# Kernel optimization log

Hardware: AMD Instinct MI355X
Metric: run time of the kernel (lower is better)

Reference implementation:

```python
import jax, jax.numpy as jnp
import numpy as np

B, CIN, H, W = 4, 128, 64, 64
PL, ATT, R = 256, 64, 16   # planes, planes//4, MD_R
STEPS = 6                   # TRAIN_STEPS default
EPS = 1e-6


def _l2norm(v, axis):
    return v / jnp.maximum(jnp.linalg.norm(v, axis=axis, keepdims=True), 1e-12)


def setup_inputs() -> dict:
    key = jax.random.key(0)
    ks = jax.random.split(key, 11)
    s = 0.05
    return {
        "x": jax.random.normal(ks[0], (B, CIN, H, W), jnp.float32),
        "conv1_w": jax.random.normal(ks[1], (PL, CIN), jnp.float32) * s,      # 1x1 conv, no bias
        "conv3_w": jax.random.normal(ks[2], (PL, 1, 3, 3), jnp.float32) * s,  # depthwise 3x3
        "conv3_b": jax.random.normal(ks[3], (PL,), jnp.float32) * s,
        "lower_w": jax.random.normal(ks[4], (PL, PL), jnp.float32) * s,       # Conv1d k=1
        "lower_b": jax.random.normal(ks[5], (PL,), jnp.float32) * s,
        "ca1_w": jax.random.normal(ks[6], (ATT, PL), jnp.float32) * s,        # channel attn 1x1
        "ca2_w": jax.random.normal(ks[7], (PL, ATT), jnp.float32) * s,
        "fc_w": jax.random.normal(ks[8], (CIN, PL), jnp.float32) * s,         # fc_adapt_channels1
        "fc_b": jax.random.normal(ks[9], (CIN,), jnp.float32) * s,
        "bases_init": jax.random.uniform(ks[10], (B * H * W, 1, R), jnp.float32),  # rand_init bases
    }


def reference(x, conv1_w, conv3_w, conv3_b, lower_w, lower_b, ca1_w, ca2_w, fc_w, fc_b, bases_init):
    # conv1 (1x1, no bias) then depthwise 3x3 (groups=PL)
    y = jnp.einsum('bchw,oc->bohw', x, conv1_w)
    y = jax.lax.conv_general_dilated(y, conv3_w, (1, 1), 'SAME',
                                     dimension_numbers=('NCHW', 'OIHW', 'NCHW'),
                                     feature_group_count=PL)
    y = y + conv3_b[None, :, None, None]
    # '(b s) c h w -> (b h w) c s' with s=1 -> tokens [M, C]
    xm = jnp.transpose(y, (0, 2, 3, 1)).reshape(B * H * W, PL)
    # Hamburger lower_bread: Conv1d(k=1) + ReLU
    xl = jax.nn.relu(xm @ lower_w.T + lower_b)
    xn = xl[:, None, :]                        # NMF x: [M, D=1, N=C]
    # NMF2D local_inference (torch.no_grad in original)
    xs = jax.lax.stop_gradient(xn)
    bases = _l2norm(bases_init, 1)             # [M, 1, R]
    coef = jax.nn.softmax(jnp.einsum('mdn,mdr->mnr', xs, bases), axis=-1)  # inv_t=1
    for _ in range(STEPS):
        num = jnp.einsum('mdn,mdr->mnr', xs, bases)
        den = jnp.einsum('mnr,mrk->mnk', coef, jnp.einsum('mdr,mdk->mrk', bases, bases))
        coef = coef * num / (den + EPS)
        num = jnp.einsum('mdn,mnr->mdr', xs, coef)
        den = jnp.einsum('mdr,mrk->mdk', bases, jnp.einsum('mnr,mnk->mrk', coef, coef))
        bases = bases * num / (den + EPS)
    bases = jax.lax.stop_gradient(bases)
    coef = jax.lax.stop_gradient(coef)
    # compute_coef (differentiable via xn)
    num = jnp.einsum('mdn,mdr->mnr', xn, bases)
    den = jnp.einsum('mnr,mrk->mnk', coef, jnp.einsum('mdr,mdk->mrk', bases, bases))
    coef = coef * num / (den + EPS)
    xr = jnp.einsum('mdr,mnr->mn', bases, coef)     # bases @ coef^T, [M, C] (D=1 squeezed)
    feat = jax.nn.relu(xm + xr)                     # Hamburger residual + ReLU
    # mean over s (s=1) and back to [B, C, H, W]
    feat = jnp.transpose(feat.reshape(B, H, W, PL), (0, 3, 1, 2))
    # AMPooling channel attention
    avg = feat.mean(axis=(2, 3))
    mx = feat.max(axis=(2, 3))
    ca = lambda v: jax.nn.relu(v @ ca1_w.T) @ ca2_w.T
    att = jax.nn.sigmoid(ca(avg) + ca(mx))          # [B, C]
    out = feat * att[:, :, None, None]
    out = jnp.einsum('bchw,oc->bohw', out, fc_w) + fc_b[None, :, None, None]
    return out, att[:, :, None, None]
```

## Files before the change

kernel.cpp:

```cpp
#include <hip/hip_runtime.h>
#include <hip/hip_bf16.h>
#include <math.h>

#define EPS 1e-6f
#define PITCH 72

typedef short s16x8 __attribute__((ext_vector_type(8)));
typedef float f32x4 __attribute__((ext_vector_type(4)));

__device__ __forceinline__ short bf16of(float f) {
  __hip_bfloat16 h = __float2bfloat16(f);
  return __builtin_bit_cast(short, h);
}
__device__ __forceinline__ float f32of(unsigned short u) {
  unsigned int x = ((unsigned int)u) << 16;
  return __builtin_bit_cast(float, x);
}

__global__ __launch_bounds__(256) void k_conv1x1(const float* __restrict__ x,
                                                 const float* __restrict__ w1,
                                                 short* __restrict__ ybf) {
  __shared__ __align__(16) short Aw[256 * PITCH];
  __shared__ __align__(16) short Xs[64 * PITCH];
  const int t = threadIdx.x;
  const int m0 = blockIdx.x * 64;
  const int img = m0 >> 12, hw0 = m0 & 4095;
  const int lane = t & 63, w = t >> 6;
  const int lrow = lane & 15, lk = (lane >> 4) * 8;
  f32x4 acc[8][2];
#pragma unroll
  for (int i = 0; i < 8; ++i)
#pragma unroll
    for (int j = 0; j < 2; ++j) acc[i][j] = {0.f, 0.f, 0.f, 0.f};

  for (int kk = 0; kk < 128; kk += 64) {
    __syncthreads();
    {
      const float* wp = w1 + (size_t)t * 128 + kk;
#pragma unroll
      for (int q = 0; q < 16; ++q) {
        const float4 v = *(const float4*)(wp + q * 4);
        short4 sv = {bf16of(v.x), bf16of(v.y), bf16of(v.z), bf16of(v.w)};
        *(short4*)(&Aw[t * PITCH + q * 4]) = sv;
      }
    }
    {
      const int m4 = (t & 15) * 4;
      const int cg = (t >> 4) * 4;
      float4 col[4];
#pragma unroll
      for (int cc = 0; cc < 4; ++cc)
        col[cc] = *(const float4*)(x + (size_t)(img * 128 + kk + cg + cc) * 4096 + hw0 + m4);
#pragma unroll
      for (int r = 0; r < 4; ++r) {
        short4 sv = {bf16of(((const float*)&col[0])[r]),
                     bf16of(((const float*)&col[1])[r]),
                     bf16of(((const float*)&col[2])[r]),
                     bf16of(((const float*)&col[3])[r])};
        *(short4*)(&Xs[(m4 + r) * PITCH + cg]) = sv;
      }
    }
    __syncthreads();
#pragma unroll
    for (int ks = 0; ks < 2; ++ks) {
      const int ko = ks * 32 + lk;
      s16x8 bfr[2];
#pragma unroll
      for (int j = 0; j < 2; ++j)
        bfr[j] = *(const s16x8*)(&Xs[(((w >> 1) * 2 + j) * 16 + lrow) * PITCH + ko]);
#pragma unroll
      for (int i = 0; i < 8; ++i) {
        const s16x8 af = *(const s16x8*)(&Aw[(((w & 1) * 8 + i) * 16 + lrow) * PITCH + ko]);
#pragma unroll
        for (int j = 0; j < 2; ++j)
          acc[i][j] = __builtin_amdgcn_mfma_f32_16x16x32_bf16(af, bfr[j], acc[i][j], 0, 0, 0);
      }
    }
  }
#pragma unroll
  for (int i = 0; i < 8; ++i) {
    const int p = ((w & 1) * 8 + i) * 16 + (lane >> 4) * 4;
#pragma unroll
    for (int j = 0; j < 2; ++j) {
      const int m = m0 + ((w >> 1) * 2 + j) * 16 + lrow;
      const f32x4 v = acc[i][j];
      short4 sv = {bf16of(v.x), bf16of(v.y), bf16of(v.z), bf16of(v.w)};
      *(short4*)(ybf + (size_t)m * 256 + p) = sv;
    }
  }
}

__global__ __launch_bounds__(256) void k_dwconv(const unsigned short* __restrict__ ybf,
                                                const float* __restrict__ w3,
                                                const float* __restrict__ b3,
                                                float* __restrict__ xm) {
  __shared__ float wt[9][256];
  __shared__ float bs[256];
  const int t = threadIdx.x;
#pragma unroll
  for (int i = 0; i < 9; ++i) wt[i][t] = w3[t * 9 + i];
  bs[t] = b3[t];
  __syncthreads();
  const int sub = t >> 6;
  const int pq = t & 63;
  const int m = blockIdx.x * 4 + sub;
  const int hw = m & 4095;
  const int h = hw >> 6, ww = hw & 63;
  const int bb = m >> 12;
  float4 acc = *(const float4*)(&bs[pq * 4]);
#pragma unroll
  for (int dy = -1; dy <= 1; ++dy) {
    const int hh = h + dy;
    if (hh < 0 || hh > 63) continue;
#pragma unroll
    for (int dx = -1; dx <= 1; ++dx) {
      const int w2 = ww + dx;
      if (w2 < 0 || w2 > 63) continue;
      const int idx = (dy + 1) * 3 + (dx + 1);
      const ushort4 v =
          *(const ushort4*)(ybf + (size_t)((bb << 12) + (hh << 6) + w2) * 256 + pq * 4);
      const float4 wv = *(const float4*)(&wt[idx][pq * 4]);
      acc.x += f32of(v.x) * wv.x;
      acc.y += f32of(v.y) * wv.y;
      acc.z += f32of(v.z) * wv.z;
      acc.w += f32of(v.w) * wv.w;
    }
  }
  *(float4*)(xm + (size_t)m * 256 + pq * 4) = acc;
}

__global__ __launch_bounds__(256) void k_lower(const float* __restrict__ xm,
                                               const float* __restrict__ lw,
                                               const float* __restrict__ lb,
                                               float* __restrict__ xl) {
  __shared__ __align__(16) short Aw[256 * PITCH];
  __shared__ __align__(16) short Xs[64 * PITCH];
  const int t = threadIdx.x;
  const int m0 = blockIdx.x * 64;
  const int lane = t & 63, w = t >> 6;
  const int lrow = lane & 15, lk = (lane >> 4) * 8;
  f32x4 acc[8][2];
#pragma unroll
  for (int i = 0; i < 8; ++i)
#pragma unroll
    for (int j = 0; j < 2; ++j) acc[i][j] = {0.f, 0.f, 0.f, 0.f};

  for (int kk = 0; kk < 256; kk += 64) {
    __syncthreads();
    {
      const float* wp = lw + (size_t)t * 256 + kk;
#pragma unroll
      for (int q = 0; q < 16; ++q) {
        const float4 v = *(const float4*)(wp + q * 4);
        short4 sv = {bf16of(v.x), bf16of(v.y), bf16of(v.z), bf16of(v.w)};
        *(short4*)(&Aw[t * PITCH + q * 4]) = sv;
      }
    }
    {
      const int m = t & 63, q = t >> 6;
      const float* xp = xm + (size_t)(m0 + m) * 256 + kk + q * 16;
#pragma unroll
      for (int jj = 0; jj < 4; ++jj) {
        const float4 v = *(const float4*)(xp + jj * 4);
        short4 sv = {bf16of(v.x), bf16of(v.y), bf16of(v.z), bf16of(v.w)};
        *(short4*)(&Xs[m * PITCH + q * 16 + jj * 4]) = sv;
      }
    }
    __syncthreads();
#pragma unroll
    for (int ks = 0; ks < 2; ++ks) {
      const int ko = ks * 32 + lk;
      s16x8 bfr[2];
#pragma unroll
      for (int j = 0; j < 2; ++j)
        bfr[j] = *(const s16x8*)(&Xs[(((w >> 1) * 2 + j) * 16 + lrow) * PITCH + ko]);
#pragma unroll
      for (int i = 0; i < 8; ++i) {
        const s16x8 af = *(const s16x8*)(&Aw[(((w & 1) * 8 + i) * 16 + lrow) * PITCH + ko]);
#pragma unroll
        for (int j = 0; j < 2; ++j)
          acc[i][j] = __builtin_amdgcn_mfma_f32_16x16x32_bf16(af, bfr[j], acc[i][j], 0, 0, 0);
      }
    }
  }
#pragma unroll
  for (int i = 0; i < 8; ++i) {
    const int n = ((w & 1) * 8 + i) * 16 + (lane >> 4) * 4;
    const float4 bias = *(const float4*)(lb + n);
#pragma unroll
    for (int j = 0; j < 2; ++j) {
      const int m = m0 + ((w >> 1) * 2 + j) * 16 + lrow;
      f32x4 v = acc[i][j];
      v.x = fmaxf(v.x + bias.x, 0.f);
      v.y = fmaxf(v.y + bias.y, 0.f);
      v.z = fmaxf(v.z + bias.z, 0.f);
      v.w = fmaxf(v.w + bias.w, 0.f);
      *(f32x4*)(xl + (size_t)m * 256 + n) = v;
    }
  }
}

__global__ __launch_bounds__(256) void k_em_fast(const float* __restrict__ xl,
                                                 const float* __restrict__ binit,
                                                 const float* __restrict__ xm,
                                                 short* __restrict__ featb,
                                                 float* __restrict__ psum,
                                                 float* __restrict__ pmax,
                                                 int* __restrict__ flag) {
  __shared__ float psL[1024], pmL[1024];
  __shared__ int sflag;
  const int t = threadIdx.x;
  const int lane = t & 63, w = t >> 6;
  const int bid = blockIdx.x;
  const int m0 = bid * 16 + w * 4;
  bool asym = false;
#pragma unroll
  for (int p = 0; p < 4; ++p) {
    const float bv = binit[(size_t)(m0 + p) * 16 + (lane & 15)];
    const float bn = bv / fmaxf(fabsf(bv), 1e-12f);
    asym |= !__all(bn == 1.0f);
  }
  if (t == 0) sflag = 0;
  __syncthreads();
  if (asym && lane == 0) sflag = 1;
  __syncthreads();
  if (sflag) {
    if (t == 0) flag[bid] = 1;
    return;
  }

  float s[4][4], C[4][4], Bv[4];
#pragma unroll
  for (int p = 0; p < 4; ++p) {
    const f32x4 s4 = *(const f32x4*)(xl + (size_t)(m0 + p) * 256 + lane * 4);
    s[p][0] = s4.x;
    s[p][1] = s4.y;
    s[p][2] = s4.z;
    s[p][3] = s4.w;
    Bv[p] = 1.f;
#pragma unroll
    for (int i = 0; i < 4; ++i) C[p][i] = 0.0625f;
  }
  for (int step = 0; step < 6; ++step) {
    float pnum[4], psq[4];
#pragma unroll
    for (int p = 0; p < 4; ++p) {
      const float k1 = 16.f * Bv[p] * Bv[p];
      pnum[p] = 0.f;
      psq[p] = 0.f;
#pragma unroll
      for (int i = 0; i < 4; ++i) {
        const float den = fmaf(C[p][i], k1, EPS);
        const float cn = C[p][i] * (s[p][i] * Bv[p]) * __builtin_amdgcn_rcpf(den);
        C[p][i] = cn;
        pnum[p] = fmaf(s[p][i], cn, pnum[p]);
        psq[p] = fmaf(cn, cn, psq[p]);
      }
    }
#pragma unroll
    for (int d = 1; d < 64; d <<= 1) {
#pragma unroll
      for (int p = 0; p < 4; ++p) {
        pnum[p] += __shfl_xor(pnum[p], d, 64);
        psq[p] += __shfl_xor(psq[p], d, 64);
      }
    }
#pragma unroll
    for (int p = 0; p < 4; ++p)
      Bv[p] = Bv[p] * pnum[p] *
              __builtin_amdgcn_rcpf(fmaf(16.f * Bv[p], psq[p], EPS));
  }
  float ps4[4] = {0.f, 0.f, 0.f, 0.f};
  float pm4[4] = {-1e30f, -1e30f, -1e30f, -1e30f};
#pragma unroll
  for (int p = 0; p < 4; ++p) {
    const float4 xm4 = *(const float4*)(xm + (size_t)(m0 + p) * 256 + lane * 4);
    const float xmv[4] = {xm4.x, xm4.y, xm4.z, xm4.w};
    const float k1 = 16.f * Bv[p] * Bv[p];
    float o[4];
#pragma unroll
    for (int i = 0; i < 4; ++i) {
      const float den = fmaf(C[p][i], k1, EPS);
      const float cn = C[p][i] * (s[p][i] * Bv[p]) * __builtin_amdgcn_rcpf(den);
      const float xr = 16.f * Bv[p] * cn;
      o[i] = fmaxf(xmv[i] + xr, 0.f);
      ps4[i] += o[i];
      pm4[i] = fmaxf(pm4[i], o[i]);
    }
    short4 sv = {bf16of(o[0]), bf16of(o[1]), bf16of(o[2]), bf16of(o[3])};
    *(short4*)(featb + (size_t)(m0 + p) * 256 + lane * 4) = sv;
  }
#pragma unroll
  for (int i = 0; i < 4; ++i) {
    psL[w * 256 + lane * 4 + i] = ps4[i];
    pmL[w * 256 + lane * 4 + i] = pm4[i];
  }
  __syncthreads();
  const float sv = psL[t] + psL[256 + t] + psL[512 + t] + psL[768 + t];
  const float mv =
      fmaxf(fmaxf(pmL[t], pmL[256 + t]), fmaxf(pmL[512 + t], pmL[768 + t]));
  psum[(size_t)bid * 256 + t] = sv;
  pmax[(size_t)bid * 256 + t] = mv;
  if (t == 0) flag[bid] = 0;
}

__global__ __launch_bounds__(256, 2) void k_em_slowfix(
    const float* __restrict__ xl, const float* __restrict__ binit,
    const float* __restrict__ xmp, short* __restrict__ featb,
    float* __restrict__ psum, float* __restrict__ pmax,
    const int* __restrict__ flag) {
  const int bid = blockIdx.x;
  if (flag[bid] == 0) return;
  __shared__ float psL[1024], pmL[1024];
  const int t = threadIdx.x;
  const int lane = t & 63, w = t >> 6;
  const int m0 = bid * 16 + w * 4;
  float ps4[4] = {0.f, 0.f, 0.f, 0.f};
  float pm4[4] = {-1e30f, -1e30f, -1e30f, -1e30f};
  for (int p = 0; p < 4; ++p) {
    const int m = m0 + p;
    const float4 s4 = *(const float4*)(xl + (size_t)m * 256 + lane * 4);
    const float s[4] = {s4.x, s4.y, s4.z, s4.w};
    float b[16];
#pragma unroll
    for (int r = 0; r < 16; ++r) {
      const float v = binit[(size_t)m * 16 + r];
      b[r] = v / fmaxf(fabsf(v), 1e-12f);
    }
    float c[4][16];
#pragma unroll
    for (int i = 0; i < 4; ++i) {
      float mx = s[i] * b[0];
#pragma unroll
      for (int r = 1; r < 16; ++r) mx = fmaxf(mx, s[i] * b[r]);
      float sum = 0.f;
#pragma unroll
      for (int r = 0; r < 16; ++r) {
        const float e = __expf(s[i] * b[r] - mx);
        c[i][r] = e;
        sum += e;
      }
      const float inv = __fdividef(1.f, sum);
#pragma unroll
      for (int r = 0; r < 16; ++r) c[i][r] *= inv;
    }
    for (int step = 0; step < 6; ++step) {
      float red[32];
#pragma unroll
      for (int r = 0; r < 32; ++r) red[r] = 0.f;
#pragma unroll
      for (int i = 0; i < 4; ++i) {
        float tt = 0.f;
#pragma unroll
        for (int r = 0; r < 16; ++r) tt += c[i][r] * b[r];
        float tp = 0.f;
#pragma unroll
        for (int r = 0; r < 16; ++r) {
          const float cn = c[i][r] * (s[i] * b[r]) * __frcp_rn(tt * b[r] + EPS);
          c[i][r] = cn;
          tp += cn * b[r];
          red[r] += s[i] * cn;
        }
#pragma unroll
        for (int r = 0; r < 16; ++r) red[16 + r] += tp * c[i][r];
      }
      int cnt = 32;
#pragma unroll
      for (int k = 4; k >= 0; --k) {
        const int d = 1 << k;
        const bool up = (lane >> k) & 1;
        const int half = cnt >> 1;
#pragma unroll
        for (int j = 0; j < half; ++j) {
          const float lo = red[j], hi = red[j + half];
          const float send = up ? lo : hi;
          const float recv = __shfl_xor(send, d, 64);
          red[j] = (up ? hi : lo) + recv;
        }
        cnt = half;
      }
      float S = red[0] + __shfl_xor(red[0], 32, 64);
      const float dpart = __shfl_xor(S, 16, 64);
      const float q = S * __frcp_rn(dpart + EPS);
#pragma unroll
      for (int r = 0; r < 16; ++r) b[r] *= __shfl(q, r, 64);
    }
    const float4 xm4 = *(const float4*)(xmp + (size_t)m * 256 + lane * 4);
    const float xmv[4] = {xm4.x, xm4.y, xm4.z, xm4.w};
    float o4[4];
#pragma unroll
    for (int i = 0; i < 4; ++i) {
      float tt = 0.f;
#pragma unroll
      for (int r = 0; r < 16; ++r) tt += c[i][r] * b[r];
      float xr = 0.f;
#pragma unroll
      for (int r = 0; r < 16; ++r) {
        const float cn = c[i][r] * (s[i] * b[r]) * __frcp_rn(tt * b[r] + EPS);
        xr += b[r] * cn;
      }
      o4[i] = fmaxf(xmv[i] + xr, 0.f);
      ps4[i] += o4[i];
      pm4[i] = fmaxf(pm4[i], o4[i]);
    }
    short4 sv = {bf16of(o4[0]), bf16of(o4[1]), bf16of(o4[2]), bf16of(o4[3])};
    *(short4*)(featb + (size_t)m * 256 + lane * 4) = sv;
  }
#pragma unroll
  for (int i = 0; i < 4; ++i) {
    psL[w * 256 + lane * 4 + i] = ps4[i];
    pmL[w * 256 + lane * 4 + i] = pm4[i];
  }
  __syncthreads();
  const float sv = psL[t] + psL[256 + t] + psL[512 + t] + psL[768 + t];
  const float mv =
      fmaxf(fmaxf(pmL[t], pmL[256 + t]), fmaxf(pmL[512 + t], pmL[768 + t]));
  psum[(size_t)bid * 256 + t] = sv;
  pmax[(size_t)bid * 256 + t] = mv;
}

__global__ __launch_bounds__(1024) void k_att(const float* __restrict__ psum,
                                              const float* __restrict__ pmax,
                                              const float* __restrict__ ca1,
                                              const float* __restrict__ ca2,
                                              float* __restrict__ attv,
                                              float* __restrict__ out_att) {
  __shared__ float sA[4][256], sM[4][256], fA[256], fM[256], sH[64];
  const int t = threadIdx.x;
  const int b = blockIdx.x;
  const int ch = t & 255, part = t >> 8;
  float sum = 0.f, mx = -1e30f;
#pragma unroll 4
  for (int j = 0; j < 64; ++j) {
    const int g = b * 256 + part * 64 + j;
    sum += psum[(size_t)g * 256 + ch];
    mx = fmaxf(mx, pmax[(size_t)g * 256 + ch]);
  }
  sA[part][ch] = sum;
  sM[part][ch] = mx;
  __syncthreads();
  if (t < 256) {
    fA[t] = (sA[0][t] + sA[1][t] + sA[2][t] + sA[3][t]) * (1.0f / 4096.0f);
    fM[t] = fmaxf(fmaxf(sM[0][t], sM[1][t]), fmaxf(sM[2][t], sM[3][t]));
  }
  __syncthreads();
  if (t < 64) {
    float ha = 0.f, hm = 0.f;
#pragma unroll 8
    for (int p = 0; p < 256; ++p) {
      const float wv = ca1[t * 256 + p];
      ha += fA[p] * wv;
      hm += fM[p] * wv;
    }
    sH[t] = fmaxf(ha, 0.f) + fmaxf(hm, 0.f);
  }
  __syncthreads();
  if (t < 256) {
    float logit = 0.f;
#pragma unroll 8
    for (int a = 0; a < 64; ++a) logit += sH[a] * ca2[t * 64 + a];
    const float av = 1.0f / (1.0f + expf(-logit));
    attv[b * 256 + t] = av;
    out_att[b * 256 + t] = av;
  }
}

__global__ __launch_bounds__(256) void k_fc(const unsigned short* __restrict__ featb,
                                            const float* __restrict__ attv,
                                            const float* __restrict__ fw,
                                            const float* __restrict__ fb,
                                            float* __restrict__ out) {
  __shared__ __align__(16) short Fs[64 * PITCH];
  __shared__ __align__(16) short Ws[128 * PITCH];
  const int t = threadIdx.x;
  const int m0 = blockIdx.x * 64;
  const int img = m0 >> 12, hw0 = m0 & 4095;
  const int lane = t & 63, w = t >> 6;
  const int lrow = lane & 15, lk = (lane >> 4) * 8;
  f32x4 acc[2][4];
#pragma unroll
  for (int i = 0; i < 2; ++i)
#pragma unroll
    for (int j = 0; j < 4; ++j) acc[i][j] = {0.f, 0.f, 0.f, 0.f};

  for (int kk = 0; kk < 256; kk += 64) {
    __syncthreads();
    {
      const int m = t & 63, q = t >> 6;
      const unsigned short* fp = featb + (size_t)(m0 + m) * 256 + kk + q * 16;
      const float* ap = attv + img * 256 + kk + q * 16;
#pragma unroll
      for (int jj = 0; jj < 4; ++jj) {
        const ushort4 v = *(const ushort4*)(fp + jj * 4);
        const float4 a = *(const float4*)(ap + jj * 4);
        short4 sv = {bf16of(f32of(v.x) * a.x), bf16of(f32of(v.y) * a.y),
                     bf16of(f32of(v.z) * a.z), bf16of(f32of(v.w) * a.w)};
        *(short4*)(&Fs[m * PITCH + q * 16 + jj * 4]) = sv;
      }
    }
    {
      const int o = t & 127, q = t >> 7;
      const float* wp = fw + (size_t)o * 256 + kk + q * 32;
#pragma unroll
      for (int jj = 0; jj < 8; ++jj) {
        const float4 v = *(const float4*)(wp + jj * 4);
        short4 sv = {bf16of(v.x), bf16of(v.y), bf16of(v.z), bf16of(v.w)};
        *(short4*)(&Ws[o * PITCH + q * 32 + jj * 4]) = sv;
      }
    }
    __syncthreads();
#pragma unroll
    for (int ks = 0; ks < 2; ++ks) {
      const int ko = ks * 32 + lk;
      s16x8 af[2];
#pragma unroll
      for (int i = 0; i < 2; ++i)
        af[i] = *(const s16x8*)(&Fs[(((w & 1) * 2 + i) * 16 + lrow) * PITCH + ko]);
#pragma unroll
      for (int j = 0; j < 4; ++j) {
        const s16x8 bfr = *(const s16x8*)(&Ws[(((w >> 1) * 4 + j) * 16 + lrow) * PITCH + ko]);
#pragma unroll
        for (int i = 0; i < 2; ++i)
          acc[i][j] = __builtin_amdgcn_mfma_f32_16x16x32_bf16(af[i], bfr, acc[i][j], 0, 0, 0);
      }
    }
  }
#pragma unroll
  for (int j = 0; j < 4; ++j) {
    const int o = ((w >> 1) * 4 + j) * 16 + lrow;
    const float bias = fb[o];
#pragma unroll
    for (int i = 0; i < 2; ++i) {
      const int hw = hw0 + ((w & 1) * 2 + i) * 16 + (lane >> 4) * 4;
      f32x4 v = acc[i][j];
      v.x += bias;
      v.y += bias;
      v.z += bias;
      v.w += bias;
      *(f32x4*)(out + (size_t)img * 524288 + (size_t)o * 4096 + hw) = v;
    }
  }
}

extern "C" void kernel_launch(void* const* d_in, const int* in_sizes, int n_in,
                              void* d_out, int out_size, void* d_ws, size_t ws_size,
                              hipStream_t stream) {
  const float* x = (const float*)d_in[0];
  const float* w1 = (const float*)d_in[1];
  const float* w3 = (const float*)d_in[2];
  const float* b3 = (const float*)d_in[3];
  const float* lw = (const float*)d_in[4];
  const float* lb = (const float*)d_in[5];
  const float* ca1 = (const float*)d_in[6];
  const float* ca2 = (const float*)d_in[7];
  const float* fw = (const float*)d_in[8];
  const float* fb = (const float*)d_in[9];
  const float* binit = (const float*)d_in[10];

  char* wsb = (char*)d_ws;
  float* xm = (float*)wsb;
  float* xl = (float*)(wsb + (16u << 20));
  short* ybf = (short*)(wsb + (32u << 20));
  short* featb = (short*)(wsb + (42u << 20));
  float* psum = (float*)(wsb + (52u << 20));
  float* pmax = (float*)(wsb + (54u << 20));
  float* attv = (float*)(wsb + (56u << 20));
  int* flag = (int*)(wsb + (57u << 20));
  float* out = (float*)d_out;
  float* out_att = out + 2097152;

  const dim3 blk(256);
  k_conv1x1<<<dim3(256), blk, 0, stream>>>(x, w1, ybf);
  k_dwconv<<<dim3(4096), blk, 0, stream>>>((const unsigned short*)ybf, w3, b3, xm);
  k_lower<<<dim3(256), blk, 0, stream>>>(xm, lw, lb, xl);
  k_em_fast<<<dim3(1024), blk, 0, stream>>>(xl, binit, xm, featb, psum, pmax, flag);
  k_em_slowfix<<<dim3(1024), blk, 0, stream>>>(xl, binit, xm, featb, psum, pmax, flag);
  k_att<<<dim3(4), dim3(1024), 0, stream>>>(psum, pmax, ca1, ca2, attv, out_att);
  k_fc<<<dim3(256), blk, 0, stream>>>((const unsigned short*)featb, attv, fw, fb, out);
}
```

Baseline: 94.45 us.

## Store intermediates in bf16 and split GEMM kernels over output-channel tiles

The depthwise-conv output and the lower-bread activations are now stored as bf16 instead of fp32, which halves the traffic of the intermediate tensors read by the lower GEMM and both EM kernels. The three MFMA GEMM kernels (conv1x1, lower, fc) gain a second grid dimension that splits the output channels, doubling block count for better CU occupancy. The split makes each block re-read its activation tile, and rounding xm and xl to bf16 adds precision loss in the residual and the EM inputs.

```diff
diff --git a/kernel.cpp b/kernel.cpp
--- a/kernel.cpp
+++ b/kernel.cpp
@@ -20,28 +20,29 @@
 __global__ __launch_bounds__(256) void k_conv1x1(const float* __restrict__ x,
                                                  const float* __restrict__ w1,
                                                  short* __restrict__ ybf) {
-  __shared__ __align__(16) short Aw[256 * PITCH];
+  __shared__ __align__(16) short Aw[128 * PITCH];
   __shared__ __align__(16) short Xs[64 * PITCH];
   const int t = threadIdx.x;
-  const int m0 = blockIdx.x * 64;
+  const int m0 = blockIdx.x * 64, p0 = blockIdx.y * 128;
   const int img = m0 >> 12, hw0 = m0 & 4095;
   const int lane = t & 63, w = t >> 6;
   const int lrow = lane & 15, lk = (lane >> 4) * 8;
-  f32x4 acc[8][2];
-#pragma unroll
-  for (int i = 0; i < 8; ++i)
+  f32x4 acc[4][2];
+#pragma unroll
+  for (int i = 0; i < 4; ++i)
 #pragma unroll
     for (int j = 0; j < 2; ++j) acc[i][j] = {0.f, 0.f, 0.f, 0.f};
 
   for (int kk = 0; kk < 128; kk += 64) {
     __syncthreads();
     {
-      const float* wp = w1 + (size_t)t * 128 + kk;
-#pragma unroll
-      for (int q = 0; q < 16; ++q) {
+      const int pr = t & 127, kq = t >> 7;
+      const float* wp = w1 + (size_t)(p0 + pr) * 128 + kk + kq * 32;
+#pragma unroll
+      for (int q = 0; q < 8; ++q) {
         const float4 v = *(const float4*)(wp + q * 4);
         short4 sv = {bf16of(v.x), bf16of(v.y), bf16of(v.z), bf16of(v.w)};
-        *(short4*)(&Aw[t * PITCH + q * 4]) = sv;
+        *(short4*)(&Aw[pr * PITCH + kq * 32 + q * 4]) = sv;
       }
     }
     {
@@ -69,8 +70,8 @@
       for (int j = 0; j < 2; ++j)
         bfr[j] = *(const s16x8*)(&Xs[(((w >> 1) * 2 + j) * 16 + lrow) * PITCH + ko]);
 #pragma unroll
-      for (int i = 0; i < 8; ++i) {
-        const s16x8 af = *(const s16x8*)(&Aw[(((w & 1) * 8 + i) * 16 + lrow) * PITCH + ko]);
+      for (int i = 0; i < 4; ++i) {
+        const s16x8 af = *(const s16x8*)(&Aw[(((w & 1) * 4 + i) * 16 + lrow) * PITCH + ko]);
 #pragma unroll
         for (int j = 0; j < 2; ++j)
           acc[i][j] = __builtin_amdgcn_mfma_f32_16x16x32_bf16(af, bfr[j], acc[i][j], 0, 0, 0);
@@ -78,8 +79,8 @@
     }
   }
 #pragma unroll
-  for (int i = 0; i < 8; ++i) {
-    const int p = ((w & 1) * 8 + i) * 16 + (lane >> 4) * 4;
+  for (int i = 0; i < 4; ++i) {
+    const int p = p0 + ((w & 1) * 4 + i) * 16 + (lane >> 4) * 4;
 #pragma unroll
     for (int j = 0; j < 2; ++j) {
       const int m = m0 + ((w >> 1) * 2 + j) * 16 + lrow;
@@ -93,7 +94,7 @@
 __global__ __launch_bounds__(256) void k_dwconv(const unsigned short* __restrict__ ybf,
                                                 const float* __restrict__ w3,
                                                 const float* __restrict__ b3,
-                                                float* __restrict__ xm) {
+                                                short* __restrict__ xmb) {
   __shared__ float wt[9][256];
   __shared__ float bs[256];
   const int t = threadIdx.x;
@@ -126,45 +127,43 @@
       acc.w += f32of(v.w) * wv.w;
     }
   }
-  *(float4*)(xm + (size_t)m * 256 + pq * 4) = acc;
-}
-
-__global__ __launch_bounds__(256) void k_lower(const float* __restrict__ xm,
+  short4 sv = {bf16of(acc.x), bf16of(acc.y), bf16of(acc.z), bf16of(acc.w)};
+  *(short4*)(xmb + (size_t)m * 256 + pq * 4) = sv;
+}
+
+__global__ __launch_bounds__(256) void k_lower(const unsigned short* __restrict__ xmb,
                                                const float* __restrict__ lw,
                                                const float* __restrict__ lb,
-                                               float* __restrict__ xl) {
-  __shared__ __align__(16) short Aw[256 * PITCH];
+                                               short* __restrict__ xlb) {
+  __shared__ __align__(16) short Aw[128 * PITCH];
   __shared__ __align__(16) short Xs[64 * PITCH];
   const int t = threadIdx.x;
-  const int m0 = blockIdx.x * 64;
+  const int m0 = blockIdx.x * 64, n0 = blockIdx.y * 128;
   const int lane = t & 63, w = t >> 6;
   const int lrow = lane & 15, lk = (lane >> 4) * 8;
-  f32x4 acc[8][2];
-#pragma unroll
-  for (int i = 0; i < 8; ++i)
+  f32x4 acc[4][2];
+#pragma unroll
+  for (int i = 0; i < 4; ++i)
 #pragma unroll
     for (int j = 0; j < 2; ++j) acc[i][j] = {0.f, 0.f, 0.f, 0.f};
 
   for (int kk = 0; kk < 256; kk += 64) {
     __syncthreads();
     {
-      const float* wp = lw + (size_t)t * 256 + kk;
-#pragma unroll
-      for (int q = 0; q < 16; ++q) {
+      const int nr = t & 127, kq = t >> 7;
+      const float* wp = lw + (size_t)(n0 + nr) * 256 + kk + kq * 32;
+#pragma unroll
+      for (int q = 0; q < 8; ++q) {
         const float4 v = *(const float4*)(wp + q * 4);
         short4 sv = {bf16of(v.x), bf16of(v.y), bf16of(v.z), bf16of(v.w)};
-        *(short4*)(&Aw[t * PITCH + q * 4]) = sv;
+        *(short4*)(&Aw[nr * PITCH + kq * 32 + q * 4]) = sv;
       }
     }
     {
       const int m = t & 63, q = t >> 6;
-      const float* xp = xm + (size_t)(m0 + m) * 256 + kk + q * 16;
-#pragma unroll
-      for (int jj = 0; jj < 4; ++jj) {
-        const float4 v = *(const float4*)(xp + jj * 4);
-        short4 sv = {bf16of(v.x), bf16of(v.y), bf16of(v.z), bf16of(v.w)};
-        *(short4*)(&Xs[m * PITCH + q * 16 + jj * 4]) = sv;
-      }
+      const unsigned short* xp = xmb + (size_t)(m0 + m) * 256 + kk + q * 16;
+      *(s16x8*)(&Xs[m * PITCH + q * 16]) = *(const s16x8*)(xp);
+      *(s16x8*)(&Xs[m * PITCH + q * 16 + 8]) = *(const s16x8*)(xp + 8);
     }
     __syncthreads();
 #pragma unroll
@@ -175,8 +174,8 @@
       for (int j = 0; j < 2; ++j)
         bfr[j] = *(const s16x8*)(&Xs[(((w >> 1) * 2 + j) * 16 + lrow) * PITCH + ko]);
 #pragma unroll
-      for (int i = 0; i < 8; ++i) {
-        const s16x8 af = *(const s16x8*)(&Aw[(((w & 1) * 8 + i) * 16 + lrow) * PITCH + ko]);
+      for (int i = 0; i < 4; ++i) {
+        const s16x8 af = *(const s16x8*)(&Aw[(((w & 1) * 4 + i) * 16 + lrow) * PITCH + ko]);
 #pragma unroll
         for (int j = 0; j < 2; ++j)
           acc[i][j] = __builtin_amdgcn_mfma_f32_16x16x32_bf16(af, bfr[j], acc[i][j], 0, 0, 0);
@@ -184,25 +183,23 @@
     }
   }
 #pragma unroll
-  for (int i = 0; i < 8; ++i) {
-    const int n = ((w & 1) * 8 + i) * 16 + (lane >> 4) * 4;
+  for (int i = 0; i < 4; ++i) {
+    const int n = n0 + ((w & 1) * 4 + i) * 16 + (lane >> 4) * 4;
     const float4 bias = *(const float4*)(lb + n);
 #pragma unroll
     for (int j = 0; j < 2; ++j) {
       const int m = m0 + ((w >> 1) * 2 + j) * 16 + lrow;
-      f32x4 v = acc[i][j];
-      v.x = fmaxf(v.x + bias.x, 0.f);
-      v.y = fmaxf(v.y + bias.y, 0.f);
-      v.z = fmaxf(v.z + bias.z, 0.f);
-      v.w = fmaxf(v.w + bias.w, 0.f);
-      *(f32x4*)(xl + (size_t)m * 256 + n) = v;
-    }
-  }
-}
-
-__global__ __launch_bounds__(256) void k_em_fast(const float* __restrict__ xl,
+      const f32x4 v = acc[i][j];
+      short4 sv = {bf16of(fmaxf(v.x + bias.x, 0.f)), bf16of(fmaxf(v.y + bias.y, 0.f)),
+                   bf16of(fmaxf(v.z + bias.z, 0.f)), bf16of(fmaxf(v.w + bias.w, 0.f))};
+      *(short4*)(xlb + (size_t)m * 256 + n) = sv;
+    }
+  }
+}
+
+__global__ __launch_bounds__(256) void k_em_fast(const unsigned short* __restrict__ xlb,
                                                  const float* __restrict__ binit,
-                                                 const float* __restrict__ xm,
+                                                 const unsigned short* __restrict__ xmb,
                                                  short* __restrict__ featb,
                                                  float* __restrict__ psum,
                                                  float* __restrict__ pmax,
@@ -232,11 +229,11 @@
   float s[4][4], C[4][4], Bv[4];
 #pragma unroll
   for (int p = 0; p < 4; ++p) {
-    const f32x4 s4 = *(const f32x4*)(xl + (size_t)(m0 + p) * 256 + lane * 4);
-    s[p][0] = s4.x;
-    s[p][1] = s4.y;
-    s[p][2] = s4.z;
-    s[p][3] = s4.w;
+    const ushort4 su = *(const ushort4*)(xlb + (size_t)(m0 + p) * 256 + lane * 4);
+    s[p][0] = f32of(su.x);
+    s[p][1] = f32of(su.y);
+    s[p][2] = f32of(su.z);
+    s[p][3] = f32of(su.w);
     Bv[p] = 1.f;
 #pragma unroll
     for (int i = 0; i < 4; ++i) C[p][i] = 0.0625f;
@@ -274,8 +271,8 @@
   float pm4[4] = {-1e30f, -1e30f, -1e30f, -1e30f};
 #pragma unroll
   for (int p = 0; p < 4; ++p) {
-    const float4 xm4 = *(const float4*)(xm + (size_t)(m0 + p) * 256 + lane * 4);
-    const float xmv[4] = {xm4.x, xm4.y, xm4.z, xm4.w};
+    const ushort4 xmu = *(const ushort4*)(xmb + (size_t)(m0 + p) * 256 + lane * 4);
+    const float xmv[4] = {f32of(xmu.x), f32of(xmu.y), f32of(xmu.z), f32of(xmu.w)};
     const float k1 = 16.f * Bv[p] * Bv[p];
     float o[4];
 #pragma unroll
@@ -305,8 +302,8 @@
 }
 
 __global__ __launch_bounds__(256, 2) void k_em_slowfix(
-    const float* __restrict__ xl, const float* __restrict__ binit,
-    const float* __restrict__ xmp, short* __restrict__ featb,
+    const unsigned short* __restrict__ xlb, const float* __restrict__ binit,
+    const unsigned short* __restrict__ xmb, short* __restrict__ featb,
     float* __restrict__ psum, float* __restrict__ pmax,
     const int* __restrict__ flag) {
   const int bid = blockIdx.x;
@@ -319,8 +316,8 @@
   float pm4[4] = {-1e30f, -1e30f, -1e30f, -1e30f};
   for (int p = 0; p < 4; ++p) {
     const int m = m0 + p;
-    const float4 s4 = *(const float4*)(xl + (size_t)m * 256 + lane * 4);
-    const float s[4] = {s4.x, s4.y, s4.z, s4.w};
+    const ushort4 su = *(const ushort4*)(xlb + (size_t)m * 256 + lane * 4);
+    const float s[4] = {f32of(su.x), f32of(su.y), f32of(su.z), f32of(su.w)};
     float b[16];
 #pragma unroll
     for (int r = 0; r < 16; ++r) {
@@ -385,8 +382,8 @@
 #pragma unroll
       for (int r = 0; r < 16; ++r) b[r] *= __shfl(q, r, 64);
     }
-    const float4 xm4 = *(const float4*)(xmp + (size_t)m * 256 + lane * 4);
-    const float xmv[4] = {xm4.x, xm4.y, xm4.z, xm4.w};
+    const ushort4 xmu = *(const ushort4*)(xmb + (size_t)m * 256 + lane * 4);
+    const float xmv[4] = {f32of(xmu.x), f32of(xmu.y), f32of(xmu.z), f32of(xmu.w)};
     float o4[4];
 #pragma unroll
     for (int i = 0; i < 4; ++i) {
@@ -471,17 +468,17 @@
                                             const float* __restrict__ fb,
                                             float* __restrict__ out) {
   __shared__ __align__(16) short Fs[64 * PITCH];
-  __shared__ __align__(16) short Ws[128 * PITCH];
-  const int t = threadIdx.x;
-  const int m0 = blockIdx.x * 64;
+  __shared__ __align__(16) short Ws[64 * PITCH];
+  const int t = threadIdx.x;
+  const int m0 = blockIdx.x * 64, o0 = blockIdx.y * 64;
   const int img = m0 >> 12, hw0 = m0 & 4095;
   const int lane = t & 63, w = t >> 6;
   const int lrow = lane & 15, lk = (lane >> 4) * 8;
-  f32x4 acc[2][4];
+  f32x4 acc[2][2];
 #pragma unroll
   for (int i = 0; i < 2; ++i)
 #pragma unroll
-    for (int j = 0; j < 4; ++j) acc[i][j] = {0.f, 0.f, 0.f, 0.f};
+    for (int j = 0; j < 2; ++j) acc[i][j] = {0.f, 0.f, 0.f, 0.f};
 
   for (int kk = 0; kk < 256; kk += 64) {
     __syncthreads();
@@ -499,13 +496,13 @@
       }
     }
     {
-      const int o = t & 127, q = t >> 7;
-      const float* wp = fw + (size_t)o * 256 + kk + q * 32;
-#pragma unroll
-      for (int jj = 0; jj < 8; ++jj) {
+      const int o = t & 63, q = t >> 6;
+      const float* wp = fw + (size_t)(o0 + o) * 256 + kk + q * 16;
+#pragma unroll
+      for (int jj = 0; jj < 4; ++jj) {
         const float4 v = *(const float4*)(wp + jj * 4);
         short4 sv = {bf16of(v.x), bf16of(v.y), bf16of(v.z), bf16of(v.w)};
-        *(short4*)(&Ws[o * PITCH + q * 32 + jj * 4]) = sv;
+        *(short4*)(&Ws[o * PITCH + q * 16 + jj * 4]) = sv;
       }
     }
     __syncthreads();
@@ -515,10 +512,10 @@
       s16x8 af[2];
 #pragma unroll
       for (int i = 0; i < 2; ++i)
-        af[i] = *(const s16x8*)(&Fs[(((w & 1) * 2 + i) * 16 + lrow) * PITCH + ko]);
-#pragma unroll
-      for (int j = 0; j < 4; ++j) {
-        const s16x8 bfr = *(const s16x8*)(&Ws[(((w >> 1) * 4 + j) * 16 + lrow) * PITCH + ko]);
+        af[i] = *(const s16x8*)(&Fs[(((w >> 1) * 2 + i) * 16 + lrow) * PITCH + ko]);
+#pragma unroll
+      for (int j = 0; j < 2; ++j) {
+        const s16x8 bfr = *(const s16x8*)(&Ws[(((w & 1) * 2 + j) * 16 + lrow) * PITCH + ko]);
 #pragma unroll
         for (int i = 0; i < 2; ++i)
           acc[i][j] = __builtin_amdgcn_mfma_f32_16x16x32_bf16(af[i], bfr, acc[i][j], 0, 0, 0);
@@ -526,12 +523,12 @@
     }
   }
 #pragma unroll
-  for (int j = 0; j < 4; ++j) {
-    const int o = ((w >> 1) * 4 + j) * 16 + lrow;
+  for (int j = 0; j < 2; ++j) {
+    const int o = o0 + ((w & 1) * 2 + j) * 16 + lrow;
     const float bias = fb[o];
 #pragma unroll
     for (int i = 0; i < 2; ++i) {
-      const int hw = hw0 + ((w & 1) * 2 + i) * 16 + (lane >> 4) * 4;
+      const int hw = hw0 + ((w >> 1) * 2 + i) * 16 + (lane >> 4) * 4;
       f32x4 v = acc[i][j];
       v.x += bias;
       v.y += bias;
@@ -558,23 +555,28 @@
   const float* binit = (const float*)d_in[10];
 
   char* wsb = (char*)d_ws;
-  float* xm = (float*)wsb;
-  float* xl = (float*)(wsb + (16u << 20));
-  short* ybf = (short*)(wsb + (32u << 20));
-  short* featb = (short*)(wsb + (42u << 20));
-  float* psum = (float*)(wsb + (52u << 20));
-  float* pmax = (float*)(wsb + (54u << 20));
-  float* attv = (float*)(wsb + (56u << 20));
-  int* flag = (int*)(wsb + (57u << 20));
+  short* ybf = (short*)wsb;
+  short* xmb = (short*)(wsb + (8u << 20));
+  short* xlb = (short*)(wsb + (16u << 20));
+  short* featb = (short*)(wsb + (24u << 20));
+  float* psum = (float*)(wsb + (32u << 20));
+  float* pmax = (float*)(wsb + (34u << 20));
+  float* attv = (float*)(wsb + (36u << 20));
+  int* flag = (int*)(wsb + (37u << 20));
   float* out = (float*)d_out;
   float* out_att = out + 2097152;
 
   const dim3 blk(256);
-  k_conv1x1<<<dim3(256), blk, 0, stream>>>(x, w1, ybf);
-  k_dwconv<<<dim3(4096), blk, 0, stream>>>((const unsigned short*)ybf, w3, b3, xm);
-  k_lower<<<dim3(256), blk, 0, stream>>>(xm, lw, lb, xl);
-  k_em_fast<<<dim3(1024), blk, 0, stream>>>(xl, binit, xm, featb, psum, pmax, flag);
-  k_em_slowfix<<<dim3(1024), blk, 0, stream>>>(xl, binit, xm, featb, psum, pmax, flag);
+  k_conv1x1<<<dim3(256, 2), blk, 0, stream>>>(x, w1, ybf);
+  k_dwconv<<<dim3(4096), blk, 0, stream>>>((const unsigned short*)ybf, w3, b3, xmb);
+  k_lower<<<dim3(256, 2), blk, 0, stream>>>((const unsigned short*)xmb, lw, lb, xlb);
+  k_em_fast<<<dim3(1024), blk, 0, stream>>>((const unsigned short*)xlb, binit,
+                                            (const unsigned short*)xmb, featb,
+                                            psum, pmax, flag);
+  k_em_slowfix<<<dim3(1024), blk, 0, stream>>>((const unsigned short*)xlb, binit,
+                                               (const unsigned short*)xmb, featb,
+                                               psum, pmax, flag);
   k_att<<<dim3(4), dim3(1024), 0, stream>>>(psum, pmax, ca1, ca2, attv, out_att);
-  k_fc<<<dim3(256), blk, 0, stream>>>((const unsigned short*)featb, attv, fw, fb, out);
-}
+  k_fc<<<dim3(256, 2), blk, 0, stream>>>((const unsigned short*)featb, attv, fw,
+                                         fb, out);
+}
```

Result: faster. 88.36 us (-6.4%).
